# Performance work log

Measured on AMD Instinct MI355X. Metric: run time of the kernel, lower is better.

The kernel has to match this reference:

```python
import jax, jax.numpy as jnp
import numpy as np

N_HARM_XYZ = 6
N_HARM_DIR = 4
HIDDEN_XYZ = 256
HIDDEN_DIR = 128
EMB_XYZ = N_HARM_XYZ * 2 * 3 + 3  # 39
EMB_DIR = N_HARM_DIR * 2 * 3 + 3  # 27


def harmonic_embedding(x, n_harmonics):
    # x: [..., 3] -> [..., n_harmonics*2*3 + 3]
    freqs = 2.0 ** jnp.arange(n_harmonics, dtype=x.dtype)  # logspace, omega0=1
    emb = (x[..., None] * freqs).reshape(*x.shape[:-1], -1)  # [..., 3*n_harm]
    return jnp.concatenate([jnp.sin(emb), jnp.cos(emb), x], axis=-1)


def setup_inputs() -> dict:
    key = jax.random.key(0)
    ks = jax.random.split(key, 32)
    R, P = 2048, 64
    inp = {
        'sample_points': jax.random.normal(ks[0], (R, P, 3), dtype=jnp.float32),
        'directions': jax.random.normal(ks[1], (R, 3), dtype=jnp.float32),
    }
    # trunk layer dims (skip concat before layer 5; last layer outputs hidden+1)
    dims_in = [EMB_XYZ, HIDDEN_XYZ, HIDDEN_XYZ, HIDDEN_XYZ, HIDDEN_XYZ,
               HIDDEN_XYZ + EMB_XYZ, HIDDEN_XYZ, HIDDEN_XYZ]
    dims_out = [HIDDEN_XYZ] * 7 + [HIDDEN_XYZ + 1]
    for i, (di, do) in enumerate(zip(dims_in, dims_out)):
        s = 1.0 / np.sqrt(di)
        inp[f'W{i}'] = jax.random.uniform(ks[2 + 2 * i], (di, do), jnp.float32, -s, s)
        inp[f'b{i}'] = jax.random.uniform(ks[3 + 2 * i], (do,), jnp.float32, -s, s)
    s = 1.0 / np.sqrt(HIDDEN_XYZ + EMB_DIR)
    inp['Wc'] = jax.random.uniform(ks[20], (HIDDEN_XYZ + EMB_DIR, HIDDEN_DIR), jnp.float32, -s, s)
    inp['bc'] = jax.random.uniform(ks[21], (HIDDEN_DIR,), jnp.float32, -s, s)
    s = 1.0 / np.sqrt(HIDDEN_DIR)
    inp['Wo'] = jax.random.uniform(ks[22], (HIDDEN_DIR, 3), jnp.float32, -s, s)
    inp['bo'] = jax.random.uniform(ks[23], (3,), jnp.float32, -s, s)
    return inp


def nerf_forward(sample_points, directions,
                 W0, b0, W1, b1, W2, b2, W3, b3, W4, b4, W5, b5, W6, b6, W7, b7,
                 Wc, bc, Wo, bo):
    R, P, _ = sample_points.shape
    pts = sample_points.reshape(-1, 3)              # [N, 3]
    e = harmonic_embedding(pts, N_HARM_XYZ)         # [N, 39]
    h = e
    # seq0: layers 0-4, ReLU after each
    for W, b in ((W0, b0), (W1, b1), (W2, b2), (W3, b3), (W4, b4)):
        h = jax.nn.relu(h @ W + b)
    # skip concat with xyz embedding, then seq1: layers 5-7 (no ReLU after last)
    h = jnp.concatenate([h, e], axis=-1)            # [N, 295]
    h = jax.nn.relu(h @ W5 + b5)
    h = jax.nn.relu(h @ W6 + b6)
    h = h @ W7 + b7                                  # [N, 257]
    sigma = jax.nn.relu(h[:, 0]).reshape(R, P, 1)
    dirs = jnp.broadcast_to(directions[:, None, :], (R, P, 3)).reshape(-1, 3)
    d = harmonic_embedding(dirs, N_HARM_DIR)         # [N, 27]
    c = jnp.concatenate([h[:, 1:], d], axis=-1)      # [N, 283]
    c = jax.nn.relu(c @ Wc + bc)
    color = jax.nn.sigmoid(c @ Wo + bo).reshape(R, P, 3)
    return color, sigma


def reference(sample_points, directions,
              W0, b0, W1, b1, W2, b2, W3, b3, W4, b4, W5, b5, W6, b6, W7, b7,
              Wc, bc, Wo, bo):
    # returns (feature, density) matching the torch dict values
    return nerf_forward(sample_points, directions,
                        W0, b0, W1, b1, W2, b2, W3, b3, W4, b4, W5, b5, W6, b6, W7, b7,
                        Wc, bc, Wo, bo)
```

## Files before the change

kernel.cpp:

```cpp
#include <hip/hip_runtime.h>

typedef __attribute__((ext_vector_type(8))) __bf16 bf16x8;
typedef __attribute__((ext_vector_type(4))) float float4_;
typedef __attribute__((ext_vector_type(4))) unsigned short ushort4_;
typedef __attribute__((ext_vector_type(8))) unsigned short ushort8_;

#define OFF_W0T 0
#define OFF_W1T 16384
#define OFF_W2T 81920
#define OFF_W3T 147456
#define OFF_W4T 212992
#define OFF_W5T 278528
#define OFF_W6T 360448
#define OFF_W7T 425984
#define OFF_WCT 491520
#define BF16_TOTAL 524288
#define WSF_BYTE_OFF (BF16_TOTAL * 2)

__device__ __forceinline__ unsigned short f2b(float v) {
  union { float f; unsigned u; } a; a.f = v;
  unsigned r = a.u + 0x7fffu + ((a.u >> 16) & 1u);
  return (unsigned short)(r >> 16);
}

__device__ __forceinline__ bf16x8 bzero() {
  union { ushort8_ u; bf16x8 b; } z;
  ushort8_ t = {0, 0, 0, 0, 0, 0, 0, 0};
  z.u = t;
  return z.b;
}

__device__ __forceinline__ ushort4_ pack4(float4_ v) {
#if __has_builtin(__builtin_amdgcn_cvt_pk_bf16_f32)
  auto p0 = __builtin_amdgcn_cvt_pk_bf16_f32(v.x, v.y);
  auto p1 = __builtin_amdgcn_cvt_pk_bf16_f32(v.z, v.w);
  union { decltype(p0) p; unsigned u; } u0, u1;
  u0.p = p0; u1.p = p1;
  ushort4_ r;
  r.x = (unsigned short)(u0.u & 0xffffu); r.y = (unsigned short)(u0.u >> 16);
  r.z = (unsigned short)(u1.u & 0xffffu); r.w = (unsigned short)(u1.u >> 16);
  return r;
#else
  ushort4_ r; r.x = f2b(v.x); r.y = f2b(v.y); r.z = f2b(v.z); r.w = f2b(v.w);
  return r;
#endif
}

__global__ __launch_bounds__(256) void prep_kernel(
    const float* __restrict__ W0, const float* __restrict__ W1,
    const float* __restrict__ W2, const float* __restrict__ W3,
    const float* __restrict__ W4, const float* __restrict__ W5,
    const float* __restrict__ W6, const float* __restrict__ W7,
    const float* __restrict__ Wc, const float* __restrict__ b7,
    unsigned short* __restrict__ wsb, float* __restrict__ wsf)
{
  int i = blockIdx.x * 256 + threadIdx.x;
  const float* src; int rs, K, n, k2, nt16; unsigned short* base;
  if (i < 8192)        { int t = i;          n = t & 255; k2 = t >> 8; src = W0; rs = 256; K = 39;  nt16 = 16; base = wsb + OFF_W0T; }
  else if (i < 139264) { int t = i - 8192;   int l = t >> 15; t &= 32767;
                         n = t & 255; k2 = t >> 8;
                         src = (l == 0) ? W1 : (l == 1) ? W2 : (l == 2) ? W3 : W4;
                         rs = 256; K = 256; nt16 = 16; base = wsb + OFF_W1T + l * 65536; }
  else if (i < 180224) { int t = i - 139264; n = t & 255; k2 = t >> 8; src = W5;     rs = 256; K = 295; nt16 = 16; base = wsb + OFF_W5T; }
  else if (i < 212992) { int t = i - 180224; n = t & 255; k2 = t >> 8; src = W6;     rs = 256; K = 256; nt16 = 16; base = wsb + OFF_W6T; }
  else if (i < 245760) { int t = i - 212992; n = t & 255; k2 = t >> 8; src = W7 + 1; rs = 257; K = 256; nt16 = 16; base = wsb + OFF_W7T; }
  else if (i < 262144) { int t = i - 245760; n = t & 127; k2 = t >> 7; src = Wc;     rs = 128; K = 256; nt16 = 8;  base = wsb + OFF_WCT; }
  else if (i < 262400) { int k = i - 262144; wsf[k] = W7[k * 257]; return; }
  else if (i < 262656) { int k = i - 262400; wsf[256 + k] = b7[k + 1]; return; }
  else return;
  const int k = k2 * 2;
  const float v0 = (k     < K) ? src[k * rs + n]       : 0.f;
  const float v1 = (k + 1 < K) ? src[(k + 1) * rs + n] : 0.f;
  const int off = ((k >> 5) * nt16 + (n >> 4)) * 512
                + ((k >> 3) & 3) * 128 + (n & 15) * 8 + (k & 7);
  const unsigned val = (unsigned)f2b(v0) | ((unsigned)f2b(v1) << 16);
  *(unsigned*)(base + off) = val;
}

template<int NT, int NTB, int KS1, int KS2, bool RELU>
__device__ __forceinline__ void layer_mm(
    const unsigned short* src1, const unsigned short* src2,
    const unsigned short* __restrict__ wT,
    const float* bias,
    unsigned short* dst, int lane, int wave)
{
  constexpr int KT = KS1 + KS2;
  const int c = lane & 15, q = lane >> 4;
  const int n0 = wave * (NT * 16);
  const unsigned short* wl = wT + (wave * NT) * 512 + lane * 8;

  float4_ acc[4][NT];
#pragma unroll
  for (int ni = 0; ni < NT; ++ni) {
    float4_ bv = *(const float4_*)(bias + n0 + ni * 16 + q * 4);
#pragma unroll
    for (int m4 = 0; m4 < 4; ++m4) acc[m4][ni] = bv;
  }

  bf16x8 aC[NT], aN[NT];
#pragma unroll
  for (int ni = 0; ni < NT; ++ni) aC[ni] = *(const bf16x8*)(wl + ni * 512);

#pragma unroll
  for (int ks = 0; ks < KT; ++ks) {
    if (ks + 1 < KT) {
#pragma unroll
      for (int ni = 0; ni < NT; ++ni)
        aN[ni] = *(const bf16x8*)(wl + ((ks + 1) * NTB + ni) * 512);
    }
#pragma unroll
    for (int mh = 0; mh < 2; ++mh) {
      bf16x8 bfr[2];
#pragma unroll
      for (int m2 = 0; m2 < 2; ++m2) {
        const int mi = mh * 2 + m2;
        if (ks < KS1) {
          bfr[m2] = *(const bf16x8*)(src1 + (ks * 4 + mi) * 512 + lane * 8);
        } else {
          const int kse = ks - KS1;
          bf16x8 ev = *(const bf16x8*)(src2 + (mi * 16 + c) * 40 + kse * 32 + q * 8);
          bfr[m2] = (kse == 0 || q == 0) ? ev : bzero();
        }
      }
#pragma unroll
      for (int ni = 0; ni < NT; ++ni)
#pragma unroll
        for (int m2 = 0; m2 < 2; ++m2)
          acc[mh * 2 + m2][ni] = __builtin_amdgcn_mfma_f32_16x16x32_bf16(
              aC[ni], bfr[m2], acc[mh * 2 + m2][ni], 0, 0, 0);
    }
    if (ks + 1 < KT) {
#pragma unroll
      for (int ni = 0; ni < NT; ++ni) aC[ni] = aN[ni];
    }
  }

  __syncthreads();
#pragma unroll
  for (int ni = 0; ni < NT; ++ni) {
    const int base = n0 + ni * 16 + q * 4;
#pragma unroll
    for (int m4 = 0; m4 < 4; ++m4) {
      float4_ v = acc[m4][ni];
      if (RELU) {
        v.x = fmaxf(v.x, 0.f); v.y = fmaxf(v.y, 0.f);
        v.z = fmaxf(v.z, 0.f); v.w = fmaxf(v.w, 0.f);
      }
      const int addr = ((base >> 5) * 4 + m4) * 512
                     + ((base >> 3) & 3) * 128 + c * 8 + (base & 7);
      *(ushort4_*)(dst + addr) = pack4(v);
    }
  }
  __syncthreads();
}

__global__ __launch_bounds__(256, 3) void nerf_kernel(
    const float* __restrict__ pts, const float* __restrict__ dirs,
    const float* __restrict__ b0, const float* __restrict__ b1,
    const float* __restrict__ b2, const float* __restrict__ b3,
    const float* __restrict__ b4, const float* __restrict__ b5,
    const float* __restrict__ b6, const float* __restrict__ b7,
    const float* __restrict__ Wc, const float* __restrict__ bc,
    const float* __restrict__ Wo, const float* __restrict__ bo,
    const unsigned short* __restrict__ wsb, const float* __restrict__ wsf,
    float* __restrict__ out)
{
  __shared__ __align__(16) unsigned short sAct[32 * 512];
  __shared__ __align__(16) unsigned short sEmb[64 * 40 + 32];
  __shared__ float s_dvec[27];
  __shared__ __align__(16) float s_biasc[128];

  const int ray = blockIdx.x;
  const int t = threadIdx.x;
  const int lane = t & 63;
  const int wave = t >> 6;

  {
    const int m = t >> 2, s4 = t & 3;
    const float* pb = pts + (ray * 64 + m) * 3;
    const float x0 = pb[0], x1 = pb[1], x2 = pb[2];
#pragma unroll
    for (int j = 0; j < 10; ++j) {
      const int cc = s4 * 10 + j;
      float v = 0.f;
      if (cc < 18) {
        const float xx = (cc < 6) ? x0 : (cc < 12) ? x1 : x2;
        v = sinf(xx * (float)(1 << (cc % 6)));
      } else if (cc < 36) {
        const int c2 = cc - 18;
        const float xx = (c2 < 6) ? x0 : (c2 < 12) ? x1 : x2;
        v = cosf(xx * (float)(1 << (c2 % 6)));
      } else if (cc == 36) v = x0;
      else if (cc == 37) v = x1;
      else if (cc == 38) v = x2;
      sEmb[m * 40 + cc] = f2b(v);
    }
  }
  if (t < 27) {
    const float* db = dirs + ray * 3;
    float v;
    if (t < 12) v = sinf(db[t >> 2] * (float)(1 << (t & 3)));
    else if (t < 24) { const int j2 = t - 12; v = cosf(db[j2 >> 2] * (float)(1 << (j2 & 3))); }
    else v = db[t - 24];
    s_dvec[t] = v;
  }
  __syncthreads();
  if (t < 128) {
    float s = bc[t];
#pragma unroll
    for (int j = 0; j < 27; ++j) s += s_dvec[j] * Wc[(256 + j) * 128 + t];
    s_biasc[t] = s;
  }

  layer_mm<4, 16, 0, 2, true >(sAct, sEmb, wsb + OFF_W0T, b0, sAct, lane, wave);
  layer_mm<4, 16, 8, 0, true >(sAct, sEmb, wsb + OFF_W1T, b1, sAct, lane, wave);
  layer_mm<4, 16, 8, 0, true >(sAct, sEmb, wsb + OFF_W2T, b2, sAct, lane, wave);
  layer_mm<4, 16, 8, 0, true >(sAct, sEmb, wsb + OFF_W3T, b3, sAct, lane, wave);
  layer_mm<4, 16, 8, 0, true >(sAct, sEmb, wsb + OFF_W4T, b4, sAct, lane, wave);
  layer_mm<4, 16, 8, 2, true >(sAct, sEmb, wsb + OFF_W5T, b5, sAct, lane, wave);
  layer_mm<4, 16, 8, 0, true >(sAct, sEmb, wsb + OFF_W6T, b6, sAct, lane, wave);

  {
    const int m = t >> 2, q4 = t & 3;
    float s = 0.f;
#pragma unroll
    for (int i8 = 0; i8 < 8; ++i8) {
      const int kb = q4 * 64 + i8 * 8;
      bf16x8 hv = *(const bf16x8*)(sAct + ((kb >> 5) * 4 + (m >> 4)) * 512
                                       + ((kb >> 3) & 3) * 128 + (m & 15) * 8);
      const float* w = wsf + kb;
#pragma unroll
      for (int j = 0; j < 8; ++j) s += (float)hv[j] * w[j];
    }
    s += __shfl_xor(s, 1); s += __shfl_xor(s, 2);
    if (q4 == 0) out[393216 + ray * 64 + m] = fmaxf(s + b7[0], 0.f);
  }

  layer_mm<4, 16, 8, 0, false>(sAct, sEmb, wsb + OFF_W7T, wsf + 256, sAct, lane, wave);
  layer_mm<2, 8,  8, 0, true >(sAct, sEmb, wsb + OFF_WCT, s_biasc, sAct, lane, wave);

  {
    const int m = t >> 2, q4 = t & 3;
    float s0 = 0.f, s1 = 0.f, s2 = 0.f;
#pragma unroll
    for (int i2 = 0; i2 < 4; ++i2) {
      const int kb = q4 * 32 + i2 * 8;
      bf16x8 cv = *(const bf16x8*)(sAct + ((kb >> 5) * 4 + (m >> 4)) * 512
                                       + ((kb >> 3) & 3) * 128 + (m & 15) * 8);
#pragma unroll
      for (int j = 0; j < 8; ++j) {
        const float cc = (float)cv[j];
        const float* w = Wo + (kb + j) * 3;
        s0 += cc * w[0]; s1 += cc * w[1]; s2 += cc * w[2];
      }
    }
    s0 += __shfl_xor(s0, 1); s0 += __shfl_xor(s0, 2);
    s1 += __shfl_xor(s1, 1); s1 += __shfl_xor(s1, 2);
    s2 += __shfl_xor(s2, 1); s2 += __shfl_xor(s2, 2);
    if (q4 == 0) {
      float* oc = out + (ray * 64 + m) * 3;
      oc[0] = 1.f / (1.f + __expf(-(s0 + bo[0])));
      oc[1] = 1.f / (1.f + __expf(-(s1 + bo[1])));
      oc[2] = 1.f / (1.f + __expf(-(s2 + bo[2])));
    }
  }
}

extern "C" void kernel_launch(void* const* d_in, const int* in_sizes, int n_in,
                              void* d_out, int out_size, void* d_ws, size_t ws_size,
                              hipStream_t stream)
{
  const float* pts  = (const float*)d_in[0];
  const float* dirs = (const float*)d_in[1];
  const float* W0 = (const float*)d_in[2];   const float* b0 = (const float*)d_in[3];
  const float* W1 = (const float*)d_in[4];   const float* b1 = (const float*)d_in[5];
  const float* W2 = (const float*)d_in[6];   const float* b2 = (const float*)d_in[7];
  const float* W3 = (const float*)d_in[8];   const float* b3 = (const float*)d_in[9];
  const float* W4 = (const float*)d_in[10];  const float* b4 = (const float*)d_in[11];
  const float* W5 = (const float*)d_in[12];  const float* b5 = (const float*)d_in[13];
  const float* W6 = (const float*)d_in[14];  const float* b6 = (const float*)d_in[15];
  const float* W7 = (const float*)d_in[16];  const float* b7 = (const float*)d_in[17];
  const float* Wc = (const float*)d_in[18];  const float* bc = (const float*)d_in[19];
  const float* Wo = (const float*)d_in[20];  const float* bo = (const float*)d_in[21];

  unsigned short* wsb = (unsigned short*)d_ws;
  float* wsf = (float*)((char*)d_ws + WSF_BYTE_OFF);

  prep_kernel<<<1026, 256, 0, stream>>>(W0, W1, W2, W3, W4, W5, W6, W7, Wc, b7, wsb, wsf);
  nerf_kernel<<<2048, 256, 0, stream>>>(pts, dirs, b0, b1, b2, b3, b4, b5, b6, b7,
                                        Wc, bc, Wo, bo, wsb, wsf, (float*)d_out);
}
```

Before: 244.0 us.

## Process two rays per 512-thread block and drop weight-fragment prefetch

Each block now handles two rays with eight waves, four per ray, and its own shared activation and embedding buffers, launching half as many blocks. The double-buffered weight register prefetch in the layer matmul is removed, and launch bounds are raised to 512 threads with a minimum of 4 blocks, to cut register pressure and raise resident waves. The bf16 conversion switches to the compiler's native __bf16 cast. Tradeoffs: block-wide __syncthreads now couple both rays, LDS use per block doubles, and weight loads are no longer overlapped with MFMA work.

```diff
diff --git a/kernel.cpp b/kernel.cpp
--- a/kernel.cpp
+++ b/kernel.cpp
@@ -17,10 +17,17 @@
 #define BF16_TOTAL 524288
 #define WSF_BYTE_OFF (BF16_TOTAL * 2)
 
+#define ACT_T 16384
+#define EMB_T 2592
+
 __device__ __forceinline__ unsigned short f2b(float v) {
   union { float f; unsigned u; } a; a.f = v;
   unsigned r = a.u + 0x7fffu + ((a.u >> 16) & 1u);
   return (unsigned short)(r >> 16);
+}
+
+__device__ __forceinline__ unsigned short f2b_hw(float v) {
+  union { __bf16 b; unsigned short u; } a; a.b = (__bf16)v; return a.u;
 }
 
 __device__ __forceinline__ bf16x8 bzero() {
@@ -31,19 +38,9 @@
 }
 
 __device__ __forceinline__ ushort4_ pack4(float4_ v) {
-#if __has_builtin(__builtin_amdgcn_cvt_pk_bf16_f32)
-  auto p0 = __builtin_amdgcn_cvt_pk_bf16_f32(v.x, v.y);
-  auto p1 = __builtin_amdgcn_cvt_pk_bf16_f32(v.z, v.w);
-  union { decltype(p0) p; unsigned u; } u0, u1;
-  u0.p = p0; u1.p = p1;
   ushort4_ r;
-  r.x = (unsigned short)(u0.u & 0xffffu); r.y = (unsigned short)(u0.u >> 16);
-  r.z = (unsigned short)(u1.u & 0xffffu); r.w = (unsigned short)(u1.u >> 16);
+  r.x = f2b_hw(v.x); r.y = f2b_hw(v.y); r.z = f2b_hw(v.z); r.w = f2b_hw(v.w);
   return r;
-#else
-  ushort4_ r; r.x = f2b(v.x); r.y = f2b(v.y); r.z = f2b(v.z); r.w = f2b(v.w);
-  return r;
-#endif
 }
 
 __global__ __launch_bounds__(256) void prep_kernel(
@@ -82,12 +79,12 @@
     const unsigned short* src1, const unsigned short* src2,
     const unsigned short* __restrict__ wT,
     const float* bias,
-    unsigned short* dst, int lane, int wave)
+    unsigned short* dst, int lane, int wq)
 {
   constexpr int KT = KS1 + KS2;
   const int c = lane & 15, q = lane >> 4;
-  const int n0 = wave * (NT * 16);
-  const unsigned short* wl = wT + (wave * NT) * 512 + lane * 8;
+  const int n0 = wq * (NT * 16);
+  const unsigned short* wl = wT + (wq * NT) * 512 + lane * 8;
 
   float4_ acc[4][NT];
 #pragma unroll
@@ -97,17 +94,12 @@
     for (int m4 = 0; m4 < 4; ++m4) acc[m4][ni] = bv;
   }
 
-  bf16x8 aC[NT], aN[NT];
-#pragma unroll
-  for (int ni = 0; ni < NT; ++ni) aC[ni] = *(const bf16x8*)(wl + ni * 512);
-
 #pragma unroll
   for (int ks = 0; ks < KT; ++ks) {
-    if (ks + 1 < KT) {
-#pragma unroll
-      for (int ni = 0; ni < NT; ++ni)
-        aN[ni] = *(const bf16x8*)(wl + ((ks + 1) * NTB + ni) * 512);
-    }
+    bf16x8 aC[NT];
+#pragma unroll
+    for (int ni = 0; ni < NT; ++ni)
+      aC[ni] = *(const bf16x8*)(wl + (ks * NTB + ni) * 512);
 #pragma unroll
     for (int mh = 0; mh < 2; ++mh) {
       bf16x8 bfr[2];
@@ -129,10 +121,6 @@
           acc[mh * 2 + m2][ni] = __builtin_amdgcn_mfma_f32_16x16x32_bf16(
               aC[ni], bfr[m2], acc[mh * 2 + m2][ni], 0, 0, 0);
     }
-    if (ks + 1 < KT) {
-#pragma unroll
-      for (int ni = 0; ni < NT; ++ni) aC[ni] = aN[ni];
-    }
   }
 
   __syncthreads();
@@ -154,7 +142,7 @@
   __syncthreads();
 }
 
-__global__ __launch_bounds__(256, 3) void nerf_kernel(
+__global__ __launch_bounds__(512, 4) void nerf_kernel(
     const float* __restrict__ pts, const float* __restrict__ dirs,
     const float* __restrict__ b0, const float* __restrict__ b1,
     const float* __restrict__ b2, const float* __restrict__ b3,
@@ -165,20 +153,22 @@
     const unsigned short* __restrict__ wsb, const float* __restrict__ wsf,
     float* __restrict__ out)
 {
-  __shared__ __align__(16) unsigned short sAct[32 * 512];
-  __shared__ __align__(16) unsigned short sEmb[64 * 40 + 32];
-  __shared__ float s_dvec[27];
-  __shared__ __align__(16) float s_biasc[128];
-
-  const int ray = blockIdx.x;
+  __shared__ __align__(16) unsigned short sAct[2 * ACT_T];
+  __shared__ __align__(16) unsigned short sEmb[2 * EMB_T];
+  __shared__ float s_dvec[2][27];
+  __shared__ float s_biasc[2][128];
+
   const int t = threadIdx.x;
   const int lane = t & 63;
   const int wave = t >> 6;
+  const int wray = wave >> 2;
+  const int wq   = wave & 3;
 
   {
     const int m = t >> 2, s4 = t & 3;
-    const float* pb = pts + (ray * 64 + m) * 3;
+    const float* pb = pts + ((long)blockIdx.x * 128 + m) * 3;
     const float x0 = pb[0], x1 = pb[1], x2 = pb[2];
+    unsigned short* er = sEmb + (m >> 6) * EMB_T + (m & 63) * 40;
 #pragma unroll
     for (int j = 0; j < 10; ++j) {
       const int cc = s4 * 10 + j;
@@ -193,60 +183,70 @@
       } else if (cc == 36) v = x0;
       else if (cc == 37) v = x1;
       else if (cc == 38) v = x2;
-      sEmb[m * 40 + cc] = f2b(v);
-    }
-  }
-  if (t < 27) {
-    const float* db = dirs + ray * 3;
+      er[cc] = f2b_hw(v);
+    }
+  }
+  if (t < 54) {
+    const int r = (t >= 27) ? 1 : 0;
+    const int j = t - 27 * r;
+    const float* db = dirs + (blockIdx.x * 2 + r) * 3;
     float v;
-    if (t < 12) v = sinf(db[t >> 2] * (float)(1 << (t & 3)));
-    else if (t < 24) { const int j2 = t - 12; v = cosf(db[j2 >> 2] * (float)(1 << (j2 & 3))); }
-    else v = db[t - 24];
-    s_dvec[t] = v;
+    if (j < 12) v = sinf(db[j >> 2] * (float)(1 << (j & 3)));
+    else if (j < 24) { const int j2 = j - 12; v = cosf(db[j2 >> 2] * (float)(1 << (j2 & 3))); }
+    else v = db[j - 24];
+    s_dvec[r][j] = v;
   }
   __syncthreads();
-  if (t < 128) {
-    float s = bc[t];
-#pragma unroll
-    for (int j = 0; j < 27; ++j) s += s_dvec[j] * Wc[(256 + j) * 128 + t];
-    s_biasc[t] = s;
-  }
-
-  layer_mm<4, 16, 0, 2, true >(sAct, sEmb, wsb + OFF_W0T, b0, sAct, lane, wave);
-  layer_mm<4, 16, 8, 0, true >(sAct, sEmb, wsb + OFF_W1T, b1, sAct, lane, wave);
-  layer_mm<4, 16, 8, 0, true >(sAct, sEmb, wsb + OFF_W2T, b2, sAct, lane, wave);
-  layer_mm<4, 16, 8, 0, true >(sAct, sEmb, wsb + OFF_W3T, b3, sAct, lane, wave);
-  layer_mm<4, 16, 8, 0, true >(sAct, sEmb, wsb + OFF_W4T, b4, sAct, lane, wave);
-  layer_mm<4, 16, 8, 2, true >(sAct, sEmb, wsb + OFF_W5T, b5, sAct, lane, wave);
-  layer_mm<4, 16, 8, 0, true >(sAct, sEmb, wsb + OFF_W6T, b6, sAct, lane, wave);
+  if (t < 256) {
+    const int r = t >> 7, cix = t & 127;
+    float s = bc[cix];
+#pragma unroll
+    for (int j = 0; j < 27; ++j) s += s_dvec[r][j] * Wc[(256 + j) * 128 + cix];
+    s_biasc[r][cix] = s;
+  }
+
+  unsigned short* rAct = sAct + wray * ACT_T;
+  const unsigned short* rEmb = sEmb + wray * EMB_T;
+
+  layer_mm<4, 16, 0, 2, true >(rAct, rEmb, wsb + OFF_W0T, b0, rAct, lane, wq);
+  layer_mm<4, 16, 8, 0, true >(rAct, rEmb, wsb + OFF_W1T, b1, rAct, lane, wq);
+  layer_mm<4, 16, 8, 0, true >(rAct, rEmb, wsb + OFF_W2T, b2, rAct, lane, wq);
+  layer_mm<4, 16, 8, 0, true >(rAct, rEmb, wsb + OFF_W3T, b3, rAct, lane, wq);
+  layer_mm<4, 16, 8, 0, true >(rAct, rEmb, wsb + OFF_W4T, b4, rAct, lane, wq);
+  layer_mm<4, 16, 8, 2, true >(rAct, rEmb, wsb + OFF_W5T, b5, rAct, lane, wq);
+  layer_mm<4, 16, 8, 0, true >(rAct, rEmb, wsb + OFF_W6T, b6, rAct, lane, wq);
 
   {
     const int m = t >> 2, q4 = t & 3;
+    const int lm = m & 63;
+    const unsigned short* hA = sAct + (m >> 6) * ACT_T;
     float s = 0.f;
 #pragma unroll
     for (int i8 = 0; i8 < 8; ++i8) {
       const int kb = q4 * 64 + i8 * 8;
-      bf16x8 hv = *(const bf16x8*)(sAct + ((kb >> 5) * 4 + (m >> 4)) * 512
-                                       + ((kb >> 3) & 3) * 128 + (m & 15) * 8);
+      bf16x8 hv = *(const bf16x8*)(hA + ((kb >> 5) * 4 + (lm >> 4)) * 512
+                                      + ((kb >> 3) & 3) * 128 + (lm & 15) * 8);
       const float* w = wsf + kb;
 #pragma unroll
       for (int j = 0; j < 8; ++j) s += (float)hv[j] * w[j];
     }
     s += __shfl_xor(s, 1); s += __shfl_xor(s, 2);
-    if (q4 == 0) out[393216 + ray * 64 + m] = fmaxf(s + b7[0], 0.f);
-  }
-
-  layer_mm<4, 16, 8, 0, false>(sAct, sEmb, wsb + OFF_W7T, wsf + 256, sAct, lane, wave);
-  layer_mm<2, 8,  8, 0, true >(sAct, sEmb, wsb + OFF_WCT, s_biasc, sAct, lane, wave);
+    if (q4 == 0) out[393216 + blockIdx.x * 128 + m] = fmaxf(s + b7[0], 0.f);
+  }
+
+  layer_mm<4, 16, 8, 0, false>(rAct, rEmb, wsb + OFF_W7T, wsf + 256, rAct, lane, wq);
+  layer_mm<2, 8,  8, 0, true >(rAct, rEmb, wsb + OFF_WCT, s_biasc[wray], rAct, lane, wq);
 
   {
     const int m = t >> 2, q4 = t & 3;
+    const int lm = m & 63;
+    const unsigned short* cA = sAct + (m >> 6) * ACT_T;
     float s0 = 0.f, s1 = 0.f, s2 = 0.f;
 #pragma unroll
     for (int i2 = 0; i2 < 4; ++i2) {
       const int kb = q4 * 32 + i2 * 8;
-      bf16x8 cv = *(const bf16x8*)(sAct + ((kb >> 5) * 4 + (m >> 4)) * 512
-                                       + ((kb >> 3) & 3) * 128 + (m & 15) * 8);
+      bf16x8 cv = *(const bf16x8*)(cA + ((kb >> 5) * 4 + (lm >> 4)) * 512
+                                      + ((kb >> 3) & 3) * 128 + (lm & 15) * 8);
 #pragma unroll
       for (int j = 0; j < 8; ++j) {
         const float cc = (float)cv[j];
@@ -258,7 +258,7 @@
     s1 += __shfl_xor(s1, 1); s1 += __shfl_xor(s1, 2);
     s2 += __shfl_xor(s2, 1); s2 += __shfl_xor(s2, 2);
     if (q4 == 0) {
-      float* oc = out + (ray * 64 + m) * 3;
+      float* oc = out + ((long)blockIdx.x * 128 + m) * 3;
       oc[0] = 1.f / (1.f + __expf(-(s0 + bo[0])));
       oc[1] = 1.f / (1.f + __expf(-(s1 + bo[1])));
       oc[2] = 1.f / (1.f + __expf(-(s2 + bo[2])));
@@ -287,6 +287,6 @@
   float* wsf = (float*)((char*)d_ws + WSF_BYTE_OFF);
 
   prep_kernel<<<1026, 256, 0, stream>>>(W0, W1, W2, W3, W4, W5, W6, W7, Wc, b7, wsb, wsf);
-  nerf_kernel<<<2048, 256, 0, stream>>>(pts, dirs, b0, b1, b2, b3, b4, b5, b6, b7,
+  nerf_kernel<<<1024, 512, 0, stream>>>(pts, dirs, b0, b1, b2, b3, b4, b5, b6, b7,
                                         Wc, bc, Wo, bo, wsb, wsf, (float*)d_out);
 }
```

Result: slower. 252.5 us (+3.5%).
